# Optimization experiments

Hardware: AMD Instinct MI355X
Metric: run time of the kernel (lower is better)

The kernel has to match this reference:

```python
import jax, jax.numpy as jnp
import numpy as np

B, N, D, P, H, DH = 1, 1536, 512, 64, 16, 64
INNER = H * DH  # 1024

def _ln(x, g, b, eps=1e-5):
    m = jnp.mean(x, axis=-1, keepdims=True)
    v = jnp.var(x, axis=-1, keepdims=True)
    return (x - m) / jnp.sqrt(v + eps) * g + b

def setup_inputs() -> dict:
    key = jax.random.key(0)
    ks = jax.random.split(key, 10)
    s = 0.02
    return {
        "node_feats": jax.random.normal(ks[0], (B, N, D), jnp.float32),
        "pair_feats": jax.random.normal(ks[1], (B, N, N, P), jnp.float32),
        "mask": jnp.ones((B, N, N), dtype=bool),
        "ln_node_g": jnp.ones((D,), jnp.float32), "ln_node_b": jnp.zeros((D,), jnp.float32),
        "ln_pair_g": jnp.ones((P,), jnp.float32), "ln_pair_b": jnp.zeros((P,), jnp.float32),
        "Wq": s * jax.random.normal(ks[2], (D, INNER), jnp.float32),
        "bq": jnp.zeros((INNER,), jnp.float32),
        "Wkv": s * jax.random.normal(ks[3], (D, 2 * INNER), jnp.float32),
        "bkv": jnp.zeros((2 * INNER,), jnp.float32),
        "qln_g": jnp.ones((INNER,), jnp.float32), "qln_b": jnp.zeros((INNER,), jnp.float32),
        "kln_g": jnp.ones((INNER,), jnp.float32), "kln_b": jnp.zeros((INNER,), jnp.float32),
        "Wg": s * jax.random.normal(ks[4], (D, INNER), jnp.float32),
        "bg": jnp.zeros((INNER,), jnp.float32),
        "Wbias": s * jax.random.normal(ks[5], (P, H), jnp.float32),
        "Wout": s * jax.random.normal(ks[6], (INNER, D), jnp.float32),
        "bout": jnp.zeros((D,), jnp.float32),
        "n_queries": 0,
        "n_keys": 0,
    }

def reference(node_feats, pair_feats, mask, ln_node_g, ln_node_b, ln_pair_g, ln_pair_b,
              Wq, bq, Wkv, bkv, qln_g, qln_b, kln_g, kln_b, Wg, bg, Wbias, Wout, bout,
              n_queries, n_keys):
    b, n, _ = node_feats.shape
    x = _ln(node_feats, ln_node_g, ln_node_b)          # [b,n,D]
    p = _ln(pair_feats, ln_pair_g, ln_pair_b)          # [b,n,n,P]
    q = _ln(x @ Wq + bq, qln_g, qln_b)                 # [b,n,I]
    kv = x @ Wkv + bkv
    k, v = jnp.split(kv, 2, axis=-1)
    k = _ln(k, kln_g, kln_b)
    g = x @ Wg + bg                                    # gating, [b,n,I]
    bias = jnp.einsum('bijp,ph->bhij', p, Wbias)       # pair bias, [b,h,n,n]
    # split heads -> [b,h,n,dh]
    split = lambda t: t.reshape(b, n, H, DH).transpose(0, 2, 1, 3)
    qh, kh, vh, gh = split(q), split(k), split(v), split(g)
    scale = DH ** -0.5
    sim = jnp.einsum('bhid,bhjd->bhij', qh, kh) * scale
    sim = jnp.where(mask[:, None, :, :], sim, jnp.finfo(sim.dtype).min)
    attn = jax.nn.softmax(sim + bias, axis=-1)
    o = jnp.einsum('bhij,bhjd->bhid', attn, vh)        # [b,h,n,dh]
    o = jax.nn.sigmoid(gh) * o
    o = o.transpose(0, 2, 1, 3).reshape(b, n, INNER)
    return o @ Wout + bout
```

## Files before the change

### kernel.cpp

```cpp
#include <hip/hip_runtime.h>

#define NN 1536
#define DD 512
#define PP 64
#define HH 16
#define DHD 64
#define INNER 1024
#define NCHUNK 4
#define JT_PER (NN / 64 / NCHUNK)

typedef __attribute__((ext_vector_type(4))) float f32x4;
typedef __attribute__((ext_vector_type(8))) _Float16 f16x8;
typedef __attribute__((ext_vector_type(4))) _Float16 f16x4;

__device__ inline float wave_sum(float v) {
#pragma unroll
  for (int m = 1; m <= 32; m <<= 1) v += __shfl_xor(v, m);
  return v;
}

__global__ __launch_bounds__(256) void prep_kernel(const float* __restrict__ Wq,
    const float* __restrict__ Wkv, const float* __restrict__ Wg,
    const float* __restrict__ Wout, const float* __restrict__ nf,
    const float* __restrict__ lng, const float* __restrict__ lnb,
    _Float16* __restrict__ BTall, _Float16* __restrict__ WoutT,
    _Float16* __restrict__ x16) {
  int bid = blockIdx.x;
  int tid = threadIdx.x;
  if (bid >= 640) {
    int i = bid - 640;
    int c = tid * 2;
    float2 v = *(const float2*)&nf[(size_t)i * DD + c];
    float s = v.x + v.y, ss = v.x * v.x + v.y * v.y;
    s = wave_sum(s); ss = wave_sum(ss);
    __shared__ float red[2][4];
    int w = tid >> 6;
    if ((tid & 63) == 0) { red[0][w] = s; red[1][w] = ss; }
    __syncthreads();
    s = red[0][0] + red[0][1] + red[0][2] + red[0][3];
    ss = red[1][0] + red[1][1] + red[1][2] + red[1][3];
    float mean = s * (1.f / DD);
    float var = ss * (1.f / DD) - mean * mean;
    float rstd = rsqrtf(var + 1e-5f);
    x16[(size_t)i * DD + c + 0] = (_Float16)((v.x - mean) * rstd * lng[c + 0] + lnb[c + 0]);
    x16[(size_t)i * DD + c + 1] = (_Float16)((v.y - mean) * rstd * lng[c + 1] + lnb[c + 1]);
    return;
  }
  const float* src; int Cs, c0, r0, outStride, outCol; _Float16* dst;
  if (bid < 512) {
    int x = bid & 63, y = bid >> 6;
    int cg0 = x * 64; r0 = y * 64;
    if (cg0 < 1024)      { src = Wq;  Cs = 1024; c0 = cg0; }
    else if (cg0 < 3072) { src = Wkv; Cs = 2048; c0 = cg0 - 1024; }
    else                 { src = Wg;  Cs = 1024; c0 = cg0 - 3072; }
    dst = BTall; outStride = DD; outCol = cg0;
  } else {
    int b = bid - 512;
    int x = b & 7, y = b >> 3;
    c0 = x * 64; r0 = y * 64;
    src = Wout; Cs = DD; dst = WoutT; outStride = INNER; outCol = c0;
  }
  __shared__ float tile[64][65];
  int ri = tid >> 4, ci = (tid & 15) * 4;
#pragma unroll
  for (int p = 0; p < 4; ++p) {
    float4 v = *(const float4*)&src[(size_t)(r0 + ri + p * 16) * Cs + c0 + ci];
    tile[ri + p * 16][ci + 0] = v.x;
    tile[ri + p * 16][ci + 1] = v.y;
    tile[ri + p * 16][ci + 2] = v.z;
    tile[ri + p * 16][ci + 3] = v.w;
  }
  __syncthreads();
  int wr = tid >> 3, wc = (tid & 7) * 8;
#pragma unroll
  for (int p = 0; p < 2; ++p) {
    f16x8 o;
#pragma unroll
    for (int jj = 0; jj < 8; ++jj) o[jj] = (_Float16)tile[wc + jj][wr + p * 32];
    *(f16x8*)&dst[(size_t)(outCol + wr + p * 32) * outStride + r0 + wc] = o;
  }
}

__global__ __launch_bounds__(256) void transpose_f16_b(const _Float16* __restrict__ in0,
    _Float16* __restrict__ out0, int R, int C) {
  const _Float16* in = in0 + (size_t)blockIdx.z * R * C;
  _Float16* out = out0 + (size_t)blockIdx.z * R * C;
  __shared__ _Float16 tile[64][72];
  int c0 = blockIdx.x * 64, r0 = blockIdx.y * 64;
  int tid = threadIdx.x;
  int ri = tid >> 3, ci = (tid & 7) * 8;
#pragma unroll
  for (int p = 0; p < 2; ++p)
    *(f16x8*)&tile[ri + p * 32][ci] = *(const f16x8*)&in[(size_t)(r0 + ri + p * 32) * C + c0 + ci];
  __syncthreads();
#pragma unroll
  for (int p = 0; p < 2; ++p) {
    f16x8 o;
#pragma unroll
    for (int jj = 0; jj < 8; ++jj) o[jj] = tile[ci + jj][ri + p * 32];
    *(f16x8*)&out[(size_t)(c0 + ri + p * 32) * R + r0 + ci] = o;
  }
}

__global__ __launch_bounds__(256) void gemm_proj(const _Float16* __restrict__ A,
    const _Float16* __restrict__ BT, const float* __restrict__ bq,
    const float* __restrict__ bkv, const float* __restrict__ bg,
    _Float16* __restrict__ C) {
  __shared__ _Float16 As[64][72];
  __shared__ _Float16 Bs[64][72];
  int tid = threadIdx.x, lane = tid & 63, w = tid >> 6;
  int m0 = blockIdx.y * 64, n0 = blockIdx.x * 64;
  int wm = (w & 1) * 32, wn = (w >> 1) * 32;
  f32x4 acc[2][2] = {};
  int r = tid >> 3, c8 = (tid & 7) * 8;
  int lr = lane & 15, lg = lane >> 4;
  for (int k0 = 0; k0 < DD; k0 += 64) {
    *(f16x8*)&As[r][c8]      = *(const f16x8*)&A[(size_t)(m0 + r) * DD + k0 + c8];
    *(f16x8*)&As[r + 32][c8] = *(const f16x8*)&A[(size_t)(m0 + r + 32) * DD + k0 + c8];
    *(f16x8*)&Bs[r][c8]      = *(const f16x8*)&BT[(size_t)(n0 + r) * DD + k0 + c8];
    *(f16x8*)&Bs[r + 32][c8] = *(const f16x8*)&BT[(size_t)(n0 + r + 32) * DD + k0 + c8];
    __syncthreads();
#pragma unroll
    for (int kf = 0; kf < 2; ++kf) {
      f16x8 a0 = *(const f16x8*)&As[wm + lr][kf * 32 + lg * 8];
      f16x8 a1 = *(const f16x8*)&As[wm + 16 + lr][kf * 32 + lg * 8];
      f16x8 b0 = *(const f16x8*)&Bs[wn + lr][kf * 32 + lg * 8];
      f16x8 b1 = *(const f16x8*)&Bs[wn + 16 + lr][kf * 32 + lg * 8];
      acc[0][0] = __builtin_amdgcn_mfma_f32_16x16x32_f16(a0, b0, acc[0][0], 0, 0, 0);
      acc[0][1] = __builtin_amdgcn_mfma_f32_16x16x32_f16(a0, b1, acc[0][1], 0, 0, 0);
      acc[1][0] = __builtin_amdgcn_mfma_f32_16x16x32_f16(a1, b0, acc[1][0], 0, 0, 0);
      acc[1][1] = __builtin_amdgcn_mfma_f32_16x16x32_f16(a1, b1, acc[1][1], 0, 0, 0);
    }
    __syncthreads();
  }
#pragma unroll
  for (int mi = 0; mi < 2; ++mi)
#pragma unroll
    for (int ni = 0; ni < 2; ++ni)
#pragma unroll
      for (int rg = 0; rg < 4; ++rg) {
        int row = m0 + wm + mi * 16 + lg * 4 + rg;
        int col = n0 + wn + ni * 16 + lr;
        float bv = (col < 1024) ? bq[col] : (col < 3072) ? bkv[col - 1024] : bg[col - 3072];
        C[(size_t)row * 4096 + col] = (_Float16)(acc[mi][ni][rg] + bv);
      }
}

__global__ __launch_bounds__(256) void gemm_f16(const _Float16* __restrict__ A,
    const _Float16* __restrict__ BT, const float* __restrict__ bias,
    float* __restrict__ C, int M, int N, int K) {
  __shared__ _Float16 As[64][72];
  __shared__ _Float16 Bs[64][72];
  int tid = threadIdx.x, lane = tid & 63, w = tid >> 6;
  int m0 = blockIdx.y * 64, n0 = blockIdx.x * 64;
  int wm = (w & 1) * 32, wn = (w >> 1) * 32;
  f32x4 acc[2][2] = {};
  int r = tid >> 3, c8 = (tid & 7) * 8;
  int lr = lane & 15, lg = lane >> 4;
  for (int k0 = 0; k0 < K; k0 += 64) {
    *(f16x8*)&As[r][c8]      = *(const f16x8*)&A[(size_t)(m0 + r) * K + k0 + c8];
    *(f16x8*)&As[r + 32][c8] = *(const f16x8*)&A[(size_t)(m0 + r + 32) * K + k0 + c8];
    *(f16x8*)&Bs[r][c8]      = *(const f16x8*)&BT[(size_t)(n0 + r) * K + k0 + c8];
    *(f16x8*)&Bs[r + 32][c8] = *(const f16x8*)&BT[(size_t)(n0 + r + 32) * K + k0 + c8];
    __syncthreads();
#pragma unroll
    for (int kf = 0; kf < 2; ++kf) {
      f16x8 a0 = *(const f16x8*)&As[wm + lr][kf * 32 + lg * 8];
      f16x8 a1 = *(const f16x8*)&As[wm + 16 + lr][kf * 32 + lg * 8];
      f16x8 b0 = *(const f16x8*)&Bs[wn + lr][kf * 32 + lg * 8];
      f16x8 b1 = *(const f16x8*)&Bs[wn + 16 + lr][kf * 32 + lg * 8];
      acc[0][0] = __builtin_amdgcn_mfma_f32_16x16x32_f16(a0, b0, acc[0][0], 0, 0, 0);
      acc[0][1] = __builtin_amdgcn_mfma_f32_16x16x32_f16(a0, b1, acc[0][1], 0, 0, 0);
      acc[1][0] = __builtin_amdgcn_mfma_f32_16x16x32_f16(a1, b0, acc[1][0], 0, 0, 0);
      acc[1][1] = __builtin_amdgcn_mfma_f32_16x16x32_f16(a1, b1, acc[1][1], 0, 0, 0);
    }
    __syncthreads();
  }
#pragma unroll
  for (int mi = 0; mi < 2; ++mi)
#pragma unroll
    for (int ni = 0; ni < 2; ++ni)
#pragma unroll
      for (int rg = 0; rg < 4; ++rg) {
        int row = m0 + wm + mi * 16 + lg * 4 + rg;
        int col = n0 + wn + ni * 16 + lr;
        C[(size_t)row * N + col] = acc[mi][ni][rg] + bias[col];
      }
}

__global__ __launch_bounds__(256) void qkv_ln_kernel(const _Float16* __restrict__ prebuf,
    const float* __restrict__ qg, const float* __restrict__ qb,
    const float* __restrict__ kg, const float* __restrict__ kb,
    _Float16* __restrict__ q16, _Float16* __restrict__ k16, _Float16* __restrict__ v16) {
  int i = blockIdx.x, tid = threadIdx.x;
  int c = tid * 4;
  const _Float16* rowp = &prebuf[(size_t)i * 4096];
  f16x4 qh = *(const f16x4*)&rowp[c];
  f16x4 kh = *(const f16x4*)&rowp[1024 + c];
  f16x4 vh = *(const f16x4*)&rowp[2048 + c];
  float qv[4], kv[4];
#pragma unroll
  for (int e = 0; e < 4; ++e) { qv[e] = (float)qh[e]; kv[e] = (float)kh[e]; }
  float qs = qv[0] + qv[1] + qv[2] + qv[3];
  float qss = qv[0] * qv[0] + qv[1] * qv[1] + qv[2] * qv[2] + qv[3] * qv[3];
  float ks = kv[0] + kv[1] + kv[2] + kv[3];
  float kss = kv[0] * kv[0] + kv[1] * kv[1] + kv[2] * kv[2] + kv[3] * kv[3];
  qs = wave_sum(qs); qss = wave_sum(qss); ks = wave_sum(ks); kss = wave_sum(kss);
  __shared__ float red[4][4];
  int w = tid >> 6;
  if ((tid & 63) == 0) { red[0][w] = qs; red[1][w] = qss; red[2][w] = ks; red[3][w] = kss; }
  __syncthreads();
  qs = red[0][0] + red[0][1] + red[0][2] + red[0][3];
  qss = red[1][0] + red[1][1] + red[1][2] + red[1][3];
  ks = red[2][0] + red[2][1] + red[2][2] + red[2][3];
  kss = red[3][0] + red[3][1] + red[3][2] + red[3][3];
  float qm = qs * (1.f / INNER), qvr = qss * (1.f / INNER) - qm * qm, qr = rsqrtf(qvr + 1e-5f);
  float km = ks * (1.f / INNER), kvr = kss * (1.f / INNER) - km * km, kr = rsqrtf(kvr + 1e-5f);
  int hh = c >> 6, d = c & 63;
  size_t off = ((size_t)hh * NN + i) * DHD + d;
  f16x4 qo, ko;
#pragma unroll
  for (int e = 0; e < 4; ++e) {
    qo[e] = (_Float16)((qv[e] - qm) * qr * qg[c + e] + qb[c + e]);
    ko[e] = (_Float16)((kv[e] - km) * kr * kg[c + e] + kb[c + e]);
  }
  *(f16x4*)&q16[off] = qo;
  *(f16x4*)&k16[off] = ko;
  *(f16x4*)&v16[off] = vh;
}

__global__ __launch_bounds__(256) void pair_bias_kernel(const float* __restrict__ pair,
    const float* __restrict__ pg, const float* __restrict__ pb,
    const float* __restrict__ Wbias, _Float16* __restrict__ bias16, int i0) {
  int i = i0 + blockIdx.x;
  int tid = threadIdx.x, lane = tid & 63, w = tid >> 6;
  int lj = lane & 15, pbase = (lane >> 4) * 8;
  f16x8 wb0, wb1;
#pragma unroll
  for (int jj = 0; jj < 8; ++jj) {
    wb0[jj] = (_Float16)Wbias[(pbase + jj) * HH + lj];
    wb1[jj] = (_Float16)Wbias[(pbase + 32 + jj) * HH + lj];
  }
  float4 g0 = *(const float4*)&pg[pbase],      g1 = *(const float4*)&pg[pbase + 4];
  float4 g2 = *(const float4*)&pg[pbase + 32], g3 = *(const float4*)&pg[pbase + 36];
  float4 b0 = *(const float4*)&pb[pbase],      b1 = *(const float4*)&pb[pbase + 4];
  float4 b2 = *(const float4*)&pb[pbase + 32], b3 = *(const float4*)&pb[pbase + 36];
  __shared__ _Float16 trans[2][16][72];
  int jbase = blockIdx.y * 256 + w * 16 + lj;
  const float* src = &pair[((size_t)i * NN + jbase) * PP];
  float4 v0 = *(const float4*)&src[pbase];
  float4 v1 = *(const float4*)&src[pbase + 4];
  float4 v2 = *(const float4*)&src[pbase + 32];
  float4 v3 = *(const float4*)&src[pbase + 36];
  for (int t4 = 0; t4 < 4; ++t4) {
    int jt0 = blockIdx.y * 256 + t4 * 64;
    float4 n0, n1, n2, n3;
    if (t4 < 3) {
      const float* nsrc = &pair[((size_t)i * NN + jbase + (t4 + 1) * 64) * PP];
      n0 = *(const float4*)&nsrc[pbase];
      n1 = *(const float4*)&nsrc[pbase + 4];
      n2 = *(const float4*)&nsrc[pbase + 32];
      n3 = *(const float4*)&nsrc[pbase + 36];
    }
    float s = v0.x + v0.y + v0.z + v0.w + v1.x + v1.y + v1.z + v1.w
            + v2.x + v2.y + v2.z + v2.w + v3.x + v3.y + v3.z + v3.w;
    float ss = v0.x * v0.x + v0.y * v0.y + v0.z * v0.z + v0.w * v0.w
             + v1.x * v1.x + v1.y * v1.y + v1.z * v1.z + v1.w * v1.w
             + v2.x * v2.x + v2.y * v2.y + v2.z * v2.z + v2.w * v2.w
             + v3.x * v3.x + v3.y * v3.y + v3.z * v3.z + v3.w * v3.w;
    s += __shfl_xor(s, 16); s += __shfl_xor(s, 32);
    ss += __shfl_xor(ss, 16); ss += __shfl_xor(ss, 32);
    float mean = s * (1.f / PP);
    float var = ss * (1.f / PP) - mean * mean;
    float rstd = rsqrtf(var + 1e-5f);
    f16x8 a0, a1;
    a0[0] = (_Float16)((v0.x - mean) * rstd * g0.x + b0.x);
    a0[1] = (_Float16)((v0.y - mean) * rstd * g0.y + b0.y);
    a0[2] = (_Float16)((v0.z - mean) * rstd * g0.z + b0.z);
    a0[3] = (_Float16)((v0.w - mean) * rstd * g0.w + b0.w);
    a0[4] = (_Float16)((v1.x - mean) * rstd * g1.x + b1.x);
    a0[5] = (_Float16)((v1.y - mean) * rstd * g1.y + b1.y);
    a0[6] = (_Float16)((v1.z - mean) * rstd * g1.z + b1.z);
    a0[7] = (_Float16)((v1.w - mean) * rstd * g1.w + b1.w);
    a1[0] = (_Float16)((v2.x - mean) * rstd * g2.x + b2.x);
    a1[1] = (_Float16)((v2.y - mean) * rstd * g2.y + b2.y);
    a1[2] = (_Float16)((v2.z - mean) * rstd * g2.z + b2.z);
    a1[3] = (_Float16)((v2.w - mean) * rstd * g2.w + b2.w);
    a1[4] = (_Float16)((v3.x - mean) * rstd * g3.x + b3.x);
    a1[5] = (_Float16)((v3.y - mean) * rstd * g3.y + b3.y);
    a1[6] = (_Float16)((v3.z - mean) * rstd * g3.z + b3.z);
    a1[7] = (_Float16)((v3.w - mean) * rstd * g3.w + b3.w);
    f32x4 cacc = {};
    cacc = __builtin_amdgcn_mfma_f32_16x16x32_f16(a0, wb0, cacc, 0, 0, 0);
    cacc = __builtin_amdgcn_mfma_f32_16x16x32_f16(a1, wb1, cacc, 0, 0, 0);
#pragma unroll
    for (int rg = 0; rg < 4; ++rg)
      trans[t4 & 1][lj][w * 16 + (lane >> 4) * 4 + rg] = (_Float16)cacc[rg];
    __syncthreads();
    int hh = tid >> 4, jc = (tid & 15) * 4;
    f16x4 ov = *(const f16x4*)&trans[t4 & 1][hh][jc];
    *(f16x4*)&bias16[((size_t)hh * NN + i) * NN + jt0 + jc] = ov;
    v0 = n0; v1 = n1; v2 = n2; v3 = n3;
  }
}

__global__ __launch_bounds__(256) void attn_kernel(const _Float16* __restrict__ q16,
    const _Float16* __restrict__ k16, const _Float16* __restrict__ vT16,
    const _Float16* __restrict__ bias16, _Float16* __restrict__ opart,
    float* __restrict__ mlbuf, int it0) {
  int it = it0 + blockIdx.x, h = blockIdx.y, ck = blockIdx.z;
  int tid = threadIdx.x, lane = tid & 63, w = tid >> 6;
  int lr = lane & 15, lg = lane >> 4;
  __shared__ _Float16 Kt[64][72];
  __shared__ _Float16 Vt[64][72];
  int ib0 = it * 64;
  int ib = ib0 + w * 16;
  f16x8 qb0 = *(const f16x8*)&q16[((size_t)h * NN + ib + lr) * DHD + lg * 8];
  f16x8 qb1 = *(const f16x8*)&q16[((size_t)h * NN + ib + lr) * DHD + 32 + lg * 8];
  float m = -INFINITY, lsum = 0.f;
  f32x4 oacc[4] = {};
  int sr = tid >> 3, sc = (tid & 7) * 8;
  int jt0g = ck * JT_PER;
  const _Float16* brow = &bias16[((size_t)h * NN + ib + lr) * NN];
  f16x8 kA, kB, vA, vB;
  {
    int j0 = jt0g * 64;
    kA = *(const f16x8*)&k16[((size_t)h * NN + j0 + sr) * DHD + sc];
    kB = *(const f16x8*)&k16[((size_t)h * NN + j0 + sr + 32) * DHD + sc];
    vA = *(const f16x8*)&vT16[((size_t)h * DHD + sr) * NN + j0 + sc];
    vB = *(const f16x8*)&vT16[((size_t)h * DHD + sr + 32) * NN + j0 + sc];
  }
  for (int jj = 0; jj < JT_PER; ++jj) {
    int j0 = (jt0g + jj) * 64;
    *(f16x8*)&Kt[sr][sc] = kA;
    *(f16x8*)&Kt[sr + 32][sc] = kB;
    *(f16x8*)&Vt[sr][sc] = vA;
    *(f16x8*)&Vt[sr + 32][sc] = vB;
    f16x4 bl[4];
#pragma unroll
    for (int jq = 0; jq < 4; ++jq)
      bl[jq] = *(const f16x4*)&brow[j0 + jq * 16 + lg * 4];
    __syncthreads();
    if (jj + 1 < JT_PER) {
      int j1 = j0 + 64;
      kA = *(const f16x8*)&k16[((size_t)h * NN + j1 + sr) * DHD + sc];
      kB = *(const f16x8*)&k16[((size_t)h * NN + j1 + sr + 32) * DHD + sc];
      vA = *(const f16x8*)&vT16[((size_t)h * DHD + sr) * NN + j1 + sc];
      vB = *(const f16x8*)&vT16[((size_t)h * DHD + sr + 32) * NN + j1 + sc];
    }
    float s[4][4];
#pragma unroll
    for (int jq = 0; jq < 4; ++jq) {
      f16x8 ka0 = *(const f16x8*)&Kt[jq * 16 + lr][lg * 8];
      f16x8 ka1 = *(const f16x8*)&Kt[jq * 16 + lr][32 + lg * 8];
      f32x4 c = {};
      c = __builtin_amdgcn_mfma_f32_16x16x32_f16(ka0, qb0, c, 0, 0, 0);
      c = __builtin_amdgcn_mfma_f32_16x16x32_f16(ka1, qb1, c, 0, 0, 0);
#pragma unroll
      for (int r = 0; r < 4; ++r)
        s[jq][r] = c[r] * 0.125f + (float)bl[jq][r];
    }
    float tmax = s[0][0];
#pragma unroll
    for (int jq = 0; jq < 4; ++jq)
#pragma unroll
      for (int r = 0; r < 4; ++r) tmax = fmaxf(tmax, s[jq][r]);
    tmax = fmaxf(tmax, __shfl_xor(tmax, 16));
    tmax = fmaxf(tmax, __shfl_xor(tmax, 32));
    float mn = fmaxf(m, tmax);
    float alpha = __expf(m - mn);
    float ps = 0.f;
    f16x4 pf[4];
#pragma unroll
    for (int jq = 0; jq < 4; ++jq)
#pragma unroll
      for (int r = 0; r < 4; ++r) {
        float p = __expf(s[jq][r] - mn);
        ps += p;
        pf[jq][r] = (_Float16)p;
      }
    ps += __shfl_xor(ps, 16);
    ps += __shfl_xor(ps, 32);
    lsum = lsum * alpha + ps;
    m = mn;
    float ar[4];
#pragma unroll
    for (int r = 0; r < 4; ++r) ar[r] = __shfl(alpha, lg * 4 + r);
#pragma unroll
    for (int dt = 0; dt < 4; ++dt)
#pragma unroll
      for (int r = 0; r < 4; ++r) oacc[dt][r] *= ar[r];
#pragma unroll
    for (int dt = 0; dt < 4; ++dt)
#pragma unroll
      for (int jq = 0; jq < 4; ++jq) {
        f16x4 vb = *(const f16x4*)&Vt[dt * 16 + lr][jq * 16 + lg * 4];
        oacc[dt] = __builtin_amdgcn_mfma_f32_16x16x16f16(pf[jq], vb, oacc[dt], 0, 0, 0);
      }
    __syncthreads();
  }
  size_t pbase = (((size_t)it * HH + h) * NCHUNK + ck) * 4096 + (size_t)w * 1024;
#pragma unroll
  for (int dt = 0; dt < 4; ++dt) {
    f16x4 ov;
#pragma unroll
    for (int r = 0; r < 4; ++r) ov[r] = (_Float16)oacc[dt][r];
    *(f16x4*)&opart[pbase + dt * 256 + lane * 4] = ov;
  }
  if (lg == 0) {
    size_t mb = (((size_t)it * HH + h) * NCHUNK + ck) * 128;
    mlbuf[mb + w * 16 + lr] = m;
    mlbuf[mb + 64 + w * 16 + lr] = lsum;
  }
}

__global__ __launch_bounds__(256) void attn_merge(const _Float16* __restrict__ opart,
    const float* __restrict__ mlbuf, const _Float16* __restrict__ prebuf,
    _Float16* __restrict__ o16) {
  int it = blockIdx.x, h = blockIdx.y;
  int tid = threadIdx.x, lane = tid & 63, w = tid >> 6;
  int lr = lane & 15, lg = lane >> 4;
  __shared__ float sm[NCHUNK][64], sl[NCHUNK][64];
  {
    int c = tid >> 6, i = tid & 63;
    size_t mb = (((size_t)it * HH + h) * NCHUNK + c) * 128;
    sm[c][i] = mlbuf[mb + i];
    sl[c][i] = mlbuf[mb + 64 + i];
  }
  __syncthreads();
  float wc[NCHUNK][4], linv[4];
#pragma unroll
  for (int r = 0; r < 4; ++r) {
    int i_loc = w * 16 + lg * 4 + r;
    float mg = sm[0][i_loc];
#pragma unroll
    for (int c = 1; c < NCHUNK; ++c) mg = fmaxf(mg, sm[c][i_loc]);
    float lt = 0.f;
#pragma unroll
    for (int c = 0; c < NCHUNK; ++c) {
      float e = __expf(sm[c][i_loc] - mg);
      wc[c][r] = e;
      lt += e * sl[c][i_loc];
    }
    linv[r] = 1.f / lt;
  }
  size_t base = ((size_t)it * HH + h) * NCHUNK * 4096 + (size_t)w * 1024;
#pragma unroll
  for (int dt = 0; dt < 4; ++dt) {
    float o[4] = {};
#pragma unroll
    for (int c = 0; c < NCHUNK; ++c) {
      f16x4 v = *(const f16x4*)&opart[base + (size_t)c * 4096 + dt * 256 + lane * 4];
#pragma unroll
      for (int r = 0; r < 4; ++r) o[r] += wc[c][r] * (float)v[r];
    }
    int d = dt * 16 + lr;
#pragma unroll
    for (int r = 0; r < 4; ++r) {
      int i = it * 64 + w * 16 + lg * 4 + r;
      float gt = (float)prebuf[(size_t)i * 4096 + 3072 + h * DHD + d];
      float val = o[r] * linv[r] * (1.f / (1.f + __expf(-gt)));
      o16[(size_t)i * INNER + h * DHD + d] = (_Float16)val;
    }
  }
}

extern "C" void kernel_launch(void* const* d_in, const int* in_sizes, int n_in,
                              void* d_out, int out_size, void* d_ws, size_t ws_size,
                              hipStream_t stream) {
  const float* node  = (const float*)d_in[0];
  const float* pair  = (const float*)d_in[1];
  const float* ln_ng = (const float*)d_in[3];
  const float* ln_nb = (const float*)d_in[4];
  const float* ln_pg = (const float*)d_in[5];
  const float* ln_pb = (const float*)d_in[6];
  const float* Wq    = (const float*)d_in[7];
  const float* bq    = (const float*)d_in[8];
  const float* Wkv   = (const float*)d_in[9];
  const float* bkv   = (const float*)d_in[10];
  const float* qlg   = (const float*)d_in[11];
  const float* qlb   = (const float*)d_in[12];
  const float* klg   = (const float*)d_in[13];
  const float* klb   = (const float*)d_in[14];
  const float* Wg    = (const float*)d_in[15];
  const float* bg    = (const float*)d_in[16];
  const float* Wbias = (const float*)d_in[17];
  const float* Wout  = (const float*)d_in[18];
  const float* bout  = (const float*)d_in[19];
  float* out = (float*)d_out;

  char* ws = (char*)d_ws;
  const size_t MB = 1u << 20;
  _Float16* BTall    = (_Float16*)(ws + 0 * MB);
  _Float16* WoutT    = (_Float16*)(ws + 4 * MB);
  _Float16* x16      = (_Float16*)(ws + 5 * MB);
  _Float16* prebuf16 = (_Float16*)(ws + 8 * MB);
  _Float16* q16      = (_Float16*)(ws + 20 * MB);
  _Float16* k16      = (_Float16*)(ws + 23 * MB);
  _Float16* v16      = (_Float16*)(ws + 26 * MB);
  _Float16* vT16     = (_Float16*)(ws + 29 * MB);
  _Float16* o16      = (_Float16*)(ws + 32 * MB);
  _Float16* bias16   = (_Float16*)(ws + 36 * MB);
  _Float16* opart    = (_Float16*)(ws + 112 * MB);
  float*    mlbuf    = (float*)(ws + 126 * MB);

  prep_kernel<<<640 + NN, 256, 0, stream>>>(Wq, Wkv, Wg, Wout, node, ln_ng, ln_nb,
                                            BTall, WoutT, x16);
  gemm_proj<<<dim3(4096 / 64, NN / 64), 256, 0, stream>>>(x16, BTall, bq, bkv, bg, prebuf16);
  qkv_ln_kernel<<<NN, 256, 0, stream>>>(prebuf16, qlg, qlb, klg, klb, q16, k16, v16);
  transpose_f16_b<<<dim3(1, NN / 64, HH), 256, 0, stream>>>(v16, vT16, NN, DHD);

  pair_bias_kernel<<<dim3(NN / 2, NN / 256), 256, 0, stream>>>(pair, ln_pg, ln_pb, Wbias, bias16, 0);
  attn_kernel<<<dim3(NN / 128, HH, NCHUNK), 256, 0, stream>>>(q16, k16, vT16, bias16, opart, mlbuf, 0);
  pair_bias_kernel<<<dim3(NN / 2, NN / 256), 256, 0, stream>>>(pair, ln_pg, ln_pb, Wbias, bias16, NN / 2);
  attn_kernel<<<dim3(NN / 128, HH, NCHUNK), 256, 0, stream>>>(q16, k16, vT16, bias16, opart, mlbuf, NN / 128);

  attn_merge<<<dim3(NN / 64, HH), 256, 0, stream>>>(opart, mlbuf, prebuf16, o16);
  gemm_f16<<<dim3(DD / 64, NN / 64), 256, 0, stream>>>(o16, WoutT, bout, out, NN, DD, INNER);
}
```

Baseline: 255.4 us.

## Fuse pair-bias computation with QKV projection GEMM into one interleaved launch

Builds one kernel whose blocks are interleaved: every seventh block runs a tile of the projection GEMM and the other six each compute one pair-bias row segment. The memory-bound pair LayerNorm/bias work is meant to overlap the compute-bound GEMM, and the split pair-bias/attention launches become a single pair-bias pass plus one attention launch. This removes several launches and the tail idle time between them. In exchange, the earlier overlap of the second pair-bias half with the first attention half is lost, and the merged kernel's shared-memory and register use is the larger of the two bodies.

```diff
diff --git a/kernel.cpp b/kernel.cpp
--- a/kernel.cpp
+++ b/kernel.cpp
@@ -81,159 +81,11 @@
   }
 }
 
-__global__ __launch_bounds__(256) void transpose_f16_b(const _Float16* __restrict__ in0,
-    _Float16* __restrict__ out0, int R, int C) {
-  const _Float16* in = in0 + (size_t)blockIdx.z * R * C;
-  _Float16* out = out0 + (size_t)blockIdx.z * R * C;
-  __shared__ _Float16 tile[64][72];
-  int c0 = blockIdx.x * 64, r0 = blockIdx.y * 64;
-  int tid = threadIdx.x;
-  int ri = tid >> 3, ci = (tid & 7) * 8;
-#pragma unroll
-  for (int p = 0; p < 2; ++p)
-    *(f16x8*)&tile[ri + p * 32][ci] = *(const f16x8*)&in[(size_t)(r0 + ri + p * 32) * C + c0 + ci];
-  __syncthreads();
-#pragma unroll
-  for (int p = 0; p < 2; ++p) {
-    f16x8 o;
-#pragma unroll
-    for (int jj = 0; jj < 8; ++jj) o[jj] = tile[ci + jj][ri + p * 32];
-    *(f16x8*)&out[(size_t)(c0 + ri + p * 32) * R + r0 + ci] = o;
-  }
-}
-
-__global__ __launch_bounds__(256) void gemm_proj(const _Float16* __restrict__ A,
-    const _Float16* __restrict__ BT, const float* __restrict__ bq,
-    const float* __restrict__ bkv, const float* __restrict__ bg,
-    _Float16* __restrict__ C) {
-  __shared__ _Float16 As[64][72];
-  __shared__ _Float16 Bs[64][72];
-  int tid = threadIdx.x, lane = tid & 63, w = tid >> 6;
-  int m0 = blockIdx.y * 64, n0 = blockIdx.x * 64;
-  int wm = (w & 1) * 32, wn = (w >> 1) * 32;
-  f32x4 acc[2][2] = {};
-  int r = tid >> 3, c8 = (tid & 7) * 8;
-  int lr = lane & 15, lg = lane >> 4;
-  for (int k0 = 0; k0 < DD; k0 += 64) {
-    *(f16x8*)&As[r][c8]      = *(const f16x8*)&A[(size_t)(m0 + r) * DD + k0 + c8];
-    *(f16x8*)&As[r + 32][c8] = *(const f16x8*)&A[(size_t)(m0 + r + 32) * DD + k0 + c8];
-    *(f16x8*)&Bs[r][c8]      = *(const f16x8*)&BT[(size_t)(n0 + r) * DD + k0 + c8];
-    *(f16x8*)&Bs[r + 32][c8] = *(const f16x8*)&BT[(size_t)(n0 + r + 32) * DD + k0 + c8];
-    __syncthreads();
-#pragma unroll
-    for (int kf = 0; kf < 2; ++kf) {
-      f16x8 a0 = *(const f16x8*)&As[wm + lr][kf * 32 + lg * 8];
-      f16x8 a1 = *(const f16x8*)&As[wm + 16 + lr][kf * 32 + lg * 8];
-      f16x8 b0 = *(const f16x8*)&Bs[wn + lr][kf * 32 + lg * 8];
-      f16x8 b1 = *(const f16x8*)&Bs[wn + 16 + lr][kf * 32 + lg * 8];
-      acc[0][0] = __builtin_amdgcn_mfma_f32_16x16x32_f16(a0, b0, acc[0][0], 0, 0, 0);
-      acc[0][1] = __builtin_amdgcn_mfma_f32_16x16x32_f16(a0, b1, acc[0][1], 0, 0, 0);
-      acc[1][0] = __builtin_amdgcn_mfma_f32_16x16x32_f16(a1, b0, acc[1][0], 0, 0, 0);
-      acc[1][1] = __builtin_amdgcn_mfma_f32_16x16x32_f16(a1, b1, acc[1][1], 0, 0, 0);
-    }
-    __syncthreads();
-  }
-#pragma unroll
-  for (int mi = 0; mi < 2; ++mi)
-#pragma unroll
-    for (int ni = 0; ni < 2; ++ni)
-#pragma unroll
-      for (int rg = 0; rg < 4; ++rg) {
-        int row = m0 + wm + mi * 16 + lg * 4 + rg;
-        int col = n0 + wn + ni * 16 + lr;
-        float bv = (col < 1024) ? bq[col] : (col < 3072) ? bkv[col - 1024] : bg[col - 3072];
-        C[(size_t)row * 4096 + col] = (_Float16)(acc[mi][ni][rg] + bv);
-      }
-}
-
-__global__ __launch_bounds__(256) void gemm_f16(const _Float16* __restrict__ A,
-    const _Float16* __restrict__ BT, const float* __restrict__ bias,
-    float* __restrict__ C, int M, int N, int K) {
-  __shared__ _Float16 As[64][72];
-  __shared__ _Float16 Bs[64][72];
-  int tid = threadIdx.x, lane = tid & 63, w = tid >> 6;
-  int m0 = blockIdx.y * 64, n0 = blockIdx.x * 64;
-  int wm = (w & 1) * 32, wn = (w >> 1) * 32;
-  f32x4 acc[2][2] = {};
-  int r = tid >> 3, c8 = (tid & 7) * 8;
-  int lr = lane & 15, lg = lane >> 4;
-  for (int k0 = 0; k0 < K; k0 += 64) {
-    *(f16x8*)&As[r][c8]      = *(const f16x8*)&A[(size_t)(m0 + r) * K + k0 + c8];
-    *(f16x8*)&As[r + 32][c8] = *(const f16x8*)&A[(size_t)(m0 + r + 32) * K + k0 + c8];
-    *(f16x8*)&Bs[r][c8]      = *(const f16x8*)&BT[(size_t)(n0 + r) * K + k0 + c8];
-    *(f16x8*)&Bs[r + 32][c8] = *(const f16x8*)&BT[(size_t)(n0 + r + 32) * K + k0 + c8];
-    __syncthreads();
-#pragma unroll
-    for (int kf = 0; kf < 2; ++kf) {
-      f16x8 a0 = *(const f16x8*)&As[wm + lr][kf * 32 + lg * 8];
-      f16x8 a1 = *(const f16x8*)&As[wm + 16 + lr][kf * 32 + lg * 8];
-      f16x8 b0 = *(const f16x8*)&Bs[wn + lr][kf * 32 + lg * 8];
-      f16x8 b1 = *(const f16x8*)&Bs[wn + 16 + lr][kf * 32 + lg * 8];
-      acc[0][0] = __builtin_amdgcn_mfma_f32_16x16x32_f16(a0, b0, acc[0][0], 0, 0, 0);
-      acc[0][1] = __builtin_amdgcn_mfma_f32_16x16x32_f16(a0, b1, acc[0][1], 0, 0, 0);
-      acc[1][0] = __builtin_amdgcn_mfma_f32_16x16x32_f16(a1, b0, acc[1][0], 0, 0, 0);
-      acc[1][1] = __builtin_amdgcn_mfma_f32_16x16x32_f16(a1, b1, acc[1][1], 0, 0, 0);
-    }
-    __syncthreads();
-  }
-#pragma unroll
-  for (int mi = 0; mi < 2; ++mi)
-#pragma unroll
-    for (int ni = 0; ni < 2; ++ni)
-#pragma unroll
-      for (int rg = 0; rg < 4; ++rg) {
-        int row = m0 + wm + mi * 16 + lg * 4 + rg;
-        int col = n0 + wn + ni * 16 + lr;
-        C[(size_t)row * N + col] = acc[mi][ni][rg] + bias[col];
-      }
-}
-
-__global__ __launch_bounds__(256) void qkv_ln_kernel(const _Float16* __restrict__ prebuf,
-    const float* __restrict__ qg, const float* __restrict__ qb,
-    const float* __restrict__ kg, const float* __restrict__ kb,
-    _Float16* __restrict__ q16, _Float16* __restrict__ k16, _Float16* __restrict__ v16) {
-  int i = blockIdx.x, tid = threadIdx.x;
-  int c = tid * 4;
-  const _Float16* rowp = &prebuf[(size_t)i * 4096];
-  f16x4 qh = *(const f16x4*)&rowp[c];
-  f16x4 kh = *(const f16x4*)&rowp[1024 + c];
-  f16x4 vh = *(const f16x4*)&rowp[2048 + c];
-  float qv[4], kv[4];
-#pragma unroll
-  for (int e = 0; e < 4; ++e) { qv[e] = (float)qh[e]; kv[e] = (float)kh[e]; }
-  float qs = qv[0] + qv[1] + qv[2] + qv[3];
-  float qss = qv[0] * qv[0] + qv[1] * qv[1] + qv[2] * qv[2] + qv[3] * qv[3];
-  float ks = kv[0] + kv[1] + kv[2] + kv[3];
-  float kss = kv[0] * kv[0] + kv[1] * kv[1] + kv[2] * kv[2] + kv[3] * kv[3];
-  qs = wave_sum(qs); qss = wave_sum(qss); ks = wave_sum(ks); kss = wave_sum(kss);
-  __shared__ float red[4][4];
-  int w = tid >> 6;
-  if ((tid & 63) == 0) { red[0][w] = qs; red[1][w] = qss; red[2][w] = ks; red[3][w] = kss; }
-  __syncthreads();
-  qs = red[0][0] + red[0][1] + red[0][2] + red[0][3];
-  qss = red[1][0] + red[1][1] + red[1][2] + red[1][3];
-  ks = red[2][0] + red[2][1] + red[2][2] + red[2][3];
-  kss = red[3][0] + red[3][1] + red[3][2] + red[3][3];
-  float qm = qs * (1.f / INNER), qvr = qss * (1.f / INNER) - qm * qm, qr = rsqrtf(qvr + 1e-5f);
-  float km = ks * (1.f / INNER), kvr = kss * (1.f / INNER) - km * km, kr = rsqrtf(kvr + 1e-5f);
-  int hh = c >> 6, d = c & 63;
-  size_t off = ((size_t)hh * NN + i) * DHD + d;
-  f16x4 qo, ko;
-#pragma unroll
-  for (int e = 0; e < 4; ++e) {
-    qo[e] = (_Float16)((qv[e] - qm) * qr * qg[c + e] + qb[c + e]);
-    ko[e] = (_Float16)((kv[e] - km) * kr * kg[c + e] + kb[c + e]);
-  }
-  *(f16x4*)&q16[off] = qo;
-  *(f16x4*)&k16[off] = ko;
-  *(f16x4*)&v16[off] = vh;
-}
-
-__global__ __launch_bounds__(256) void pair_bias_kernel(const float* __restrict__ pair,
-    const float* __restrict__ pg, const float* __restrict__ pb,
-    const float* __restrict__ Wbias, _Float16* __restrict__ bias16, int i0) {
-  int i = i0 + blockIdx.x;
-  int tid = threadIdx.x, lane = tid & 63, w = tid >> 6;
+__device__ __forceinline__ void pb_body(int i, int jy, int tid,
+    const float* __restrict__ pair, const float* __restrict__ pg,
+    const float* __restrict__ pb, const float* __restrict__ Wbias,
+    _Float16* __restrict__ bias16) {
+  int lane = tid & 63, w = tid >> 6;
   int lj = lane & 15, pbase = (lane >> 4) * 8;
   f16x8 wb0, wb1;
 #pragma unroll
@@ -246,14 +98,14 @@
   float4 b0 = *(const float4*)&pb[pbase],      b1 = *(const float4*)&pb[pbase + 4];
   float4 b2 = *(const float4*)&pb[pbase + 32], b3 = *(const float4*)&pb[pbase + 36];
   __shared__ _Float16 trans[2][16][72];
-  int jbase = blockIdx.y * 256 + w * 16 + lj;
+  int jbase = jy * 256 + w * 16 + lj;
   const float* src = &pair[((size_t)i * NN + jbase) * PP];
   float4 v0 = *(const float4*)&src[pbase];
   float4 v1 = *(const float4*)&src[pbase + 4];
   float4 v2 = *(const float4*)&src[pbase + 32];
   float4 v3 = *(const float4*)&src[pbase + 36];
   for (int t4 = 0; t4 < 4; ++t4) {
-    int jt0 = blockIdx.y * 256 + t4 * 64;
+    int jt0 = jy * 256 + t4 * 64;
     float4 n0, n1, n2, n3;
     if (t4 < 3) {
       const float* nsrc = &pair[((size_t)i * NN + jbase + (t4 + 1) * 64) * PP];
@@ -304,11 +156,177 @@
   }
 }
 
+__device__ __forceinline__ void gemm_proj_body(int m0, int n0, int tid,
+    const _Float16* __restrict__ A, const _Float16* __restrict__ BT,
+    const float* __restrict__ bq, const float* __restrict__ bkv,
+    const float* __restrict__ bg, _Float16* __restrict__ C) {
+  __shared__ _Float16 As[64][72];
+  __shared__ _Float16 Bs[64][72];
+  int lane = tid & 63, w = tid >> 6;
+  int wm = (w & 1) * 32, wn = (w >> 1) * 32;
+  f32x4 acc[2][2] = {};
+  int r = tid >> 3, c8 = (tid & 7) * 8;
+  int lr = lane & 15, lg = lane >> 4;
+  for (int k0 = 0; k0 < DD; k0 += 64) {
+    *(f16x8*)&As[r][c8]      = *(const f16x8*)&A[(size_t)(m0 + r) * DD + k0 + c8];
+    *(f16x8*)&As[r + 32][c8] = *(const f16x8*)&A[(size_t)(m0 + r + 32) * DD + k0 + c8];
+    *(f16x8*)&Bs[r][c8]      = *(const f16x8*)&BT[(size_t)(n0 + r) * DD + k0 + c8];
+    *(f16x8*)&Bs[r + 32][c8] = *(const f16x8*)&BT[(size_t)(n0 + r + 32) * DD + k0 + c8];
+    __syncthreads();
+#pragma unroll
+    for (int kf = 0; kf < 2; ++kf) {
+      f16x8 a0 = *(const f16x8*)&As[wm + lr][kf * 32 + lg * 8];
+      f16x8 a1 = *(const f16x8*)&As[wm + 16 + lr][kf * 32 + lg * 8];
+      f16x8 b0 = *(const f16x8*)&Bs[wn + lr][kf * 32 + lg * 8];
+      f16x8 b1 = *(const f16x8*)&Bs[wn + 16 + lr][kf * 32 + lg * 8];
+      acc[0][0] = __builtin_amdgcn_mfma_f32_16x16x32_f16(a0, b0, acc[0][0], 0, 0, 0);
+      acc[0][1] = __builtin_amdgcn_mfma_f32_16x16x32_f16(a0, b1, acc[0][1], 0, 0, 0);
+      acc[1][0] = __builtin_amdgcn_mfma_f32_16x16x32_f16(a1, b0, acc[1][0], 0, 0, 0);
+      acc[1][1] = __builtin_amdgcn_mfma_f32_16x16x32_f16(a1, b1, acc[1][1], 0, 0, 0);
+    }
+    __syncthreads();
+  }
+#pragma unroll
+  for (int mi = 0; mi < 2; ++mi)
+#pragma unroll
+    for (int ni = 0; ni < 2; ++ni)
+#pragma unroll
+      for (int rg = 0; rg < 4; ++rg) {
+        int row = m0 + wm + mi * 16 + lg * 4 + rg;
+        int col = n0 + wn + ni * 16 + lr;
+        float bv = (col < 1024) ? bq[col] : (col < 3072) ? bkv[col - 1024] : bg[col - 3072];
+        C[(size_t)row * 4096 + col] = (_Float16)(acc[mi][ni][rg] + bv);
+      }
+}
+
+__global__ __launch_bounds__(256) void fat_pb_gemm(const float* __restrict__ pair,
+    const float* __restrict__ pg, const float* __restrict__ pb,
+    const float* __restrict__ Wbias, _Float16* __restrict__ bias16,
+    const _Float16* __restrict__ x16, const _Float16* __restrict__ BTall,
+    const float* __restrict__ bq, const float* __restrict__ bkv,
+    const float* __restrict__ bg, _Float16* __restrict__ prebuf16) {
+  int bid = blockIdx.x;
+  int g = bid / 7, r = bid - g * 7;
+  int tid = threadIdx.x;
+  if (r == 6) {
+    gemm_proj_body((g >> 6) * 64, (g & 63) * 64, tid, x16, BTall, bq, bkv, bg, prebuf16);
+  } else {
+    int p = g * 6 + r;
+    int jy = p / NN;
+    int i = p - jy * NN;
+    pb_body(i, jy, tid, pair, pg, pb, Wbias, bias16);
+  }
+}
+
+__global__ __launch_bounds__(256) void transpose_f16_b(const _Float16* __restrict__ in0,
+    _Float16* __restrict__ out0, int R, int C) {
+  const _Float16* in = in0 + (size_t)blockIdx.z * R * C;
+  _Float16* out = out0 + (size_t)blockIdx.z * R * C;
+  __shared__ _Float16 tile[64][72];
+  int c0 = blockIdx.x * 64, r0 = blockIdx.y * 64;
+  int tid = threadIdx.x;
+  int ri = tid >> 3, ci = (tid & 7) * 8;
+#pragma unroll
+  for (int p = 0; p < 2; ++p)
+    *(f16x8*)&tile[ri + p * 32][ci] = *(const f16x8*)&in[(size_t)(r0 + ri + p * 32) * C + c0 + ci];
+  __syncthreads();
+#pragma unroll
+  for (int p = 0; p < 2; ++p) {
+    f16x8 o;
+#pragma unroll
+    for (int jj = 0; jj < 8; ++jj) o[jj] = tile[ci + jj][ri + p * 32];
+    *(f16x8*)&out[(size_t)(c0 + ri + p * 32) * R + r0 + ci] = o;
+  }
+}
+
+__global__ __launch_bounds__(256) void gemm_f16(const _Float16* __restrict__ A,
+    const _Float16* __restrict__ BT, const float* __restrict__ bias,
+    float* __restrict__ C, int M, int N, int K) {
+  __shared__ _Float16 As[64][72];
+  __shared__ _Float16 Bs[64][72];
+  int tid = threadIdx.x, lane = tid & 63, w = tid >> 6;
+  int m0 = blockIdx.y * 64, n0 = blockIdx.x * 64;
+  int wm = (w & 1) * 32, wn = (w >> 1) * 32;
+  f32x4 acc[2][2] = {};
+  int r = tid >> 3, c8 = (tid & 7) * 8;
+  int lr = lane & 15, lg = lane >> 4;
+  for (int k0 = 0; k0 < K; k0 += 64) {
+    *(f16x8*)&As[r][c8]      = *(const f16x8*)&A[(size_t)(m0 + r) * K + k0 + c8];
+    *(f16x8*)&As[r + 32][c8] = *(const f16x8*)&A[(size_t)(m0 + r + 32) * K + k0 + c8];
+    *(f16x8*)&Bs[r][c8]      = *(const f16x8*)&BT[(size_t)(n0 + r) * K + k0 + c8];
+    *(f16x8*)&Bs[r + 32][c8] = *(const f16x8*)&BT[(size_t)(n0 + r + 32) * K + k0 + c8];
+    __syncthreads();
+#pragma unroll
+    for (int kf = 0; kf < 2; ++kf) {
+      f16x8 a0 = *(const f16x8*)&As[wm + lr][kf * 32 + lg * 8];
+      f16x8 a1 = *(const f16x8*)&As[wm + 16 + lr][kf * 32 + lg * 8];
+      f16x8 b0 = *(const f16x8*)&Bs[wn + lr][kf * 32 + lg * 8];
+      f16x8 b1 = *(const f16x8*)&Bs[wn + 16 + lr][kf * 32 + lg * 8];
+      acc[0][0] = __builtin_amdgcn_mfma_f32_16x16x32_f16(a0, b0, acc[0][0], 0, 0, 0);
+      acc[0][1] = __builtin_amdgcn_mfma_f32_16x16x32_f16(a0, b1, acc[0][1], 0, 0, 0);
+      acc[1][0] = __builtin_amdgcn_mfma_f32_16x16x32_f16(a1, b0, acc[1][0], 0, 0, 0);
+      acc[1][1] = __builtin_amdgcn_mfma_f32_16x16x32_f16(a1, b1, acc[1][1], 0, 0, 0);
+    }
+    __syncthreads();
+  }
+#pragma unroll
+  for (int mi = 0; mi < 2; ++mi)
+#pragma unroll
+    for (int ni = 0; ni < 2; ++ni)
+#pragma unroll
+      for (int rg = 0; rg < 4; ++rg) {
+        int row = m0 + wm + mi * 16 + lg * 4 + rg;
+        int col = n0 + wn + ni * 16 + lr;
+        C[(size_t)row * N + col] = acc[mi][ni][rg] + bias[col];
+      }
+}
+
+__global__ __launch_bounds__(256) void qkv_ln_kernel(const _Float16* __restrict__ prebuf,
+    const float* __restrict__ qg, const float* __restrict__ qb,
+    const float* __restrict__ kg, const float* __restrict__ kb,
+    _Float16* __restrict__ q16, _Float16* __restrict__ k16, _Float16* __restrict__ v16) {
+  int i = blockIdx.x, tid = threadIdx.x;
+  int c = tid * 4;
+  const _Float16* rowp = &prebuf[(size_t)i * 4096];
+  f16x4 qh = *(const f16x4*)&rowp[c];
+  f16x4 kh = *(const f16x4*)&rowp[1024 + c];
+  f16x4 vh = *(const f16x4*)&rowp[2048 + c];
+  float qv[4], kv[4];
+#pragma unroll
+  for (int e = 0; e < 4; ++e) { qv[e] = (float)qh[e]; kv[e] = (float)kh[e]; }
+  float qs = qv[0] + qv[1] + qv[2] + qv[3];
+  float qss = qv[0] * qv[0] + qv[1] * qv[1] + qv[2] * qv[2] + qv[3] * qv[3];
+  float ks = kv[0] + kv[1] + kv[2] + kv[3];
+  float kss = kv[0] * kv[0] + kv[1] * kv[1] + kv[2] * kv[2] + kv[3] * kv[3];
+  qs = wave_sum(qs); qss = wave_sum(qss); ks = wave_sum(ks); kss = wave_sum(kss);
+  __shared__ float red[4][4];
+  int w = tid >> 6;
+  if ((tid & 63) == 0) { red[0][w] = qs; red[1][w] = qss; red[2][w] = ks; red[3][w] = kss; }
+  __syncthreads();
+  qs = red[0][0] + red[0][1] + red[0][2] + red[0][3];
+  qss = red[1][0] + red[1][1] + red[1][2] + red[1][3];
+  ks = red[2][0] + red[2][1] + red[2][2] + red[2][3];
+  kss = red[3][0] + red[3][1] + red[3][2] + red[3][3];
+  float qm = qs * (1.f / INNER), qvr = qss * (1.f / INNER) - qm * qm, qr = rsqrtf(qvr + 1e-5f);
+  float km = ks * (1.f / INNER), kvr = kss * (1.f / INNER) - km * km, kr = rsqrtf(kvr + 1e-5f);
+  int hh = c >> 6, d = c & 63;
+  size_t off = ((size_t)hh * NN + i) * DHD + d;
+  f16x4 qo, ko;
+#pragma unroll
+  for (int e = 0; e < 4; ++e) {
+    qo[e] = (_Float16)((qv[e] - qm) * qr * qg[c + e] + qb[c + e]);
+    ko[e] = (_Float16)((kv[e] - km) * kr * kg[c + e] + kb[c + e]);
+  }
+  *(f16x4*)&q16[off] = qo;
+  *(f16x4*)&k16[off] = ko;
+  *(f16x4*)&v16[off] = vh;
+}
+
 __global__ __launch_bounds__(256) void attn_kernel(const _Float16* __restrict__ q16,
     const _Float16* __restrict__ k16, const _Float16* __restrict__ vT16,
     const _Float16* __restrict__ bias16, _Float16* __restrict__ opart,
-    float* __restrict__ mlbuf, int it0) {
-  int it = it0 + blockIdx.x, h = blockIdx.y, ck = blockIdx.z;
+    float* __restrict__ mlbuf) {
+  int it = blockIdx.x, h = blockIdx.y, ck = blockIdx.z;
   int tid = threadIdx.x, lane = tid & 63, w = tid >> 6;
   int lr = lane & 15, lg = lane >> 4;
   __shared__ _Float16 Kt[64][72];
@@ -506,15 +524,11 @@
 
   prep_kernel<<<640 + NN, 256, 0, stream>>>(Wq, Wkv, Wg, Wout, node, ln_ng, ln_nb,
                                             BTall, WoutT, x16);
-  gemm_proj<<<dim3(4096 / 64, NN / 64), 256, 0, stream>>>(x16, BTall, bq, bkv, bg, prebuf16);
+  fat_pb_gemm<<<10752, 256, 0, stream>>>(pair, ln_pg, ln_pb, Wbias, bias16,
+                                         x16, BTall, bq, bkv, bg, prebuf16);
   qkv_ln_kernel<<<NN, 256, 0, stream>>>(prebuf16, qlg, qlb, klg, klb, q16, k16, v16);
   transpose_f16_b<<<dim3(1, NN / 64, HH), 256, 0, stream>>>(v16, vT16, NN, DHD);
-
-  pair_bias_kernel<<<dim3(NN / 2, NN / 256), 256, 0, stream>>>(pair, ln_pg, ln_pb, Wbias, bias16, 0);
-  attn_kernel<<<dim3(NN / 128, HH, NCHUNK), 256, 0, stream>>>(q16, k16, vT16, bias16, opart, mlbuf, 0);
-  pair_bias_kernel<<<dim3(NN / 2, NN / 256), 256, 0, stream>>>(pair, ln_pg, ln_pb, Wbias, bias16, NN / 2);
-  attn_kernel<<<dim3(NN / 128, HH, NCHUNK), 256, 0, stream>>>(q16, k16, vT16, bias16, opart, mlbuf, NN / 128);
-
+  attn_kernel<<<dim3(NN / 64, HH, NCHUNK), 256, 0, stream>>>(q16, k16, vT16, bias16, opart, mlbuf);
   attn_merge<<<dim3(NN / 64, HH), 256, 0, stream>>>(opart, mlbuf, prebuf16, o16);
   gemm_f16<<<dim3(DD / 64, NN / 64), 256, 0, stream>>>(o16, WoutT, bout, out, NN, DD, INNER);
 }
```

Measured after the change: 239.6 us, median of 2. -6.2%, faster.
